# Performance work log

Hardware: AMD Instinct MI355X
Metric: run time of the kernel (lower is better)

Reference implementation:

```python
import jax, jax.numpy as jnp
import numpy as np
import math

N_H = 16
REL_K = 16  # relative-position clamp window


def setup_inputs() -> dict:
    key = jax.random.key(0)
    ks = jax.random.split(key, 7)
    B, S, D = 8, 1024, 1024
    d_k = D // N_H
    scale = 0.02
    return {
        "x": jax.random.normal(ks[0], (B, S, D), dtype=jnp.float32),
        "W_attn": jax.random.normal(ks[1], (D, 3 * D), dtype=jnp.float32) * scale,
        "b_attn": jax.random.normal(ks[2], (3 * D,), dtype=jnp.float32) * scale,
        "W_proj": jax.random.normal(ks[3], (D, D), dtype=jnp.float32) * scale,
        "b_proj": jax.random.normal(ks[4], (D,), dtype=jnp.float32) * scale,
        "lut_k": jax.random.normal(ks[5], (2 * REL_K + 1, d_k), dtype=jnp.float32) * scale,
        "lut_v": jax.random.normal(ks[6], (2 * REL_K + 1, d_k), dtype=jnp.float32) * scale,
    }


def reference(x, W_attn, b_attn, W_proj, b_proj, lut_k, lut_v):
    B, S, D = x.shape
    d_k = D // N_H

    qkv = x @ W_attn + b_attn  # [B, S, 3D]
    q, k, v = jnp.split(qkv, 3, axis=-1)
    # [B, H, S, d_k]
    q = q.reshape(B, S, N_H, d_k).transpose(0, 2, 1, 3)
    k = k.reshape(B, S, N_H, d_k).transpose(0, 2, 1, 3)
    v = v.reshape(B, S, N_H, d_k).transpose(0, 2, 1, 3)

    i = jnp.arange(S)[:, None]
    j = jnp.arange(S)[None, :]
    rel = jnp.clip(j - i, -REL_K, REL_K) + REL_K  # [S, S] in [0, 2k]
    aij_k = lut_k[rel]  # [S, S, d_k]
    aij_v = lut_v[rel]  # [S, S, d_k]

    scores = jnp.einsum('bhid,bhjd->bhij', q, k)
    scores = scores + jnp.einsum('bhid,ijd->bhij', q, aij_k)
    scores = scores * (1.0 / math.sqrt(d_k))

    causal = j <= i  # [S, S]
    scores = jnp.where(causal[None, None, :, :], scores, -jnp.inf)
    attn = jax.nn.softmax(scores, axis=-1)  # [B, H, S, S]

    out = jnp.einsum('bhij,bhjd->bhid', attn, v)
    out = out + jnp.einsum('bhij,ijd->bhid', attn, aij_v)
    out = out.transpose(0, 2, 1, 3).reshape(B, S, D)
    return out @ W_proj + b_proj
```

## Files before the change

### kernel.cpp

```cpp
#include <hip/hip_runtime.h>
#include <hip/hip_bf16.h>
#include <math.h>

#define NH 16
#define S_LEN 1024
#define DK 64
#define D_MODEL 1024
#define HSZ 8388608

typedef __attribute__((ext_vector_type(8))) short bf16x8;
typedef __attribute__((ext_vector_type(4))) float f32x4;
typedef unsigned short USH;

#define EXPSCALE 0.1803368801111204f

__device__ __forceinline__ float fast_exp2(float x) {
    return __builtin_amdgcn_exp2f(x);
}

__device__ __forceinline__ short f2b(float x) {
    union { __hip_bfloat16 h; short s; } u;
    u.h = __float2bfloat16(x);
    return u.s;
}
__device__ __forceinline__ float b2f(USH u) {
    union { unsigned i; float f; } x;
    x.i = (unsigned)u << 16;
    return x.f;
}

__device__ __forceinline__ void gload16(const void* src, void* lds) {
    __builtin_amdgcn_global_load_lds(
        (const __attribute__((address_space(1))) void*)src,
        (__attribute__((address_space(3))) void*)lds,
        16, 0, 0);
}

__global__ __launch_bounds__(256)
void conv_bf16_kernel(const float* __restrict__ in, USH* __restrict__ out) {
    const int i = (blockIdx.x * 256 + threadIdx.x) * 8;
    const float4 a = *(const float4*)&in[i];
    const float4 b = *(const float4*)&in[i + 4];
    ushort4 o0, o1;
    o0.x = (USH)f2b(a.x); o0.y = (USH)f2b(a.y); o0.z = (USH)f2b(a.z); o0.w = (USH)f2b(a.w);
    o1.x = (USH)f2b(b.x); o1.y = (USH)f2b(b.y); o1.z = (USH)f2b(b.z); o1.w = (USH)f2b(b.w);
    *(ushort4*)&out[i] = o0;
    *(ushort4*)&out[i + 4] = o1;
}

__global__ __launch_bounds__(256)
void transp_bf16_kernel(const float* __restrict__ in, USH* __restrict__ out,
                        int R, int C) {
    __shared__ USH Ts[64][65];
    const int r0 = blockIdx.y * 64, c0 = blockIdx.x * 64;
    const int tr = threadIdx.x >> 4;
    const int tc4 = (threadIdx.x & 15) * 4;
    #pragma unroll
    for (int ph = 0; ph < 4; ++ph) {
        const int r = ph * 16 + tr;
        const float4 v = *(const float4*)&in[(size_t)(r0 + r) * C + c0 + tc4];
        Ts[tc4 + 0][r] = (USH)f2b(v.x);
        Ts[tc4 + 1][r] = (USH)f2b(v.y);
        Ts[tc4 + 2][r] = (USH)f2b(v.z);
        Ts[tc4 + 3][r] = (USH)f2b(v.w);
    }
    __syncthreads();
    #pragma unroll
    for (int ph = 0; ph < 4; ++ph) {
        const int cc = ph * 16 + tr;
        ushort4 o;
        o.x = Ts[cc][tc4 + 0]; o.y = Ts[cc][tc4 + 1];
        o.z = Ts[cc][tc4 + 2]; o.w = Ts[cc][tc4 + 3];
        *(ushort4*)&out[(size_t)(c0 + cc) * R + r0 + tc4] = o;
    }
}

__global__ __launch_bounds__(256)
void vtransp_kernel(const USH* __restrict__ in, USH* __restrict__ out) {
    __shared__ USH T[64][72];
    const int bh = blockIdx.x >> 4;
    const int s0 = (blockIdx.x & 15) * 64;
    const int r = threadIdx.x >> 4;
    const int c4 = (threadIdx.x & 15) * 4;
    #pragma unroll
    for (int ph = 0; ph < 4; ++ph) {
        const int row = ph * 16 + r;
        const ushort4 v = *(const ushort4*)
            &in[((size_t)bh * S_LEN + s0 + row) * DK + c4];
        T[row][c4 + 0] = v.x; T[row][c4 + 1] = v.y;
        T[row][c4 + 2] = v.z; T[row][c4 + 3] = v.w;
    }
    __syncthreads();
    #pragma unroll
    for (int ph = 0; ph < 4; ++ph) {
        const int d = ph * 16 + r;
        ushort4 o;
        o.x = T[c4 + 0][d]; o.y = T[c4 + 1][d];
        o.z = T[c4 + 2][d]; o.w = T[c4 + 3][d];
        *(ushort4*)&out[(size_t)bh * (S_LEN * DK) + (size_t)d * S_LEN + s0 + c4] = o;
    }
}

template<int QKV>
__global__ __launch_bounds__(256)
void mfma_gemm_kernel(const USH* __restrict__ A, const USH* __restrict__ Bt,
                      const float* __restrict__ bias,
                      float* __restrict__ Cf, USH* __restrict__ Cq,
                      USH* __restrict__ Ck, USH* __restrict__ Cv,
                      int M, int N, int K) {
    __shared__ __align__(16) USH As[128 * 32];
    __shared__ __align__(16) USH Bs[128 * 32];
    const int t = threadIdx.x;
    const int w = t >> 6, lane = t & 63, g = lane >> 4, c = lane & 15;
    const int wm = w >> 1, wn = w & 1;
    const int bm0 = blockIdx.y * 128, bn0 = blockIdx.x * 128;

    const int sk = ((t & 3) ^ ((t >> 3) & 3)) * 8;
    const USH* pa0 = A + (size_t)(bm0 + (t >> 2)) * K + sk;
    const USH* pa1 = pa0 + (size_t)64 * K;
    const USH* pb0 = Bt + (size_t)(bn0 + (t >> 2)) * K + sk;
    const USH* pb1 = pb0 + (size_t)64 * K;
    USH* ldsA0 = &As[(t & ~63) * 8];
    USH* ldsA1 = ldsA0 + 2048;
    USH* ldsB0 = &Bs[(t & ~63) * 8];
    USH* ldsB1 = ldsB0 + 2048;

    unsigned aoff[4], boff[4];
    #pragma unroll
    for (int i = 0; i < 4; ++i) {
        const int r = wm * 64 + i * 16 + c;
        aoff[i] = ((unsigned)(r * 64 + g * 16)) ^ ((((unsigned)r >> 1) & 3) << 4);
        const int n = wn * 64 + i * 16 + c;
        boff[i] = ((unsigned)(n * 64 + g * 16)) ^ ((((unsigned)n >> 1) & 3) << 4);
    }

    f32x4 acc[4][4];
    #pragma unroll
    for (int i = 0; i < 4; ++i)
        #pragma unroll
        for (int j = 0; j < 4; ++j) acc[i][j] = (f32x4)0.f;

    for (int k0 = 0; k0 < K; k0 += 32) {
        gload16(pa0 + k0, ldsA0);
        gload16(pa1 + k0, ldsA1);
        gload16(pb0 + k0, ldsB0);
        gload16(pb1 + k0, ldsB1);
        __syncthreads();

        bf16x8 af[4], bfr[4];
        #pragma unroll
        for (int i = 0; i < 4; ++i) af[i] = *(const bf16x8*)((const char*)As + aoff[i]);
        #pragma unroll
        for (int j = 0; j < 4; ++j) bfr[j] = *(const bf16x8*)((const char*)Bs + boff[j]);
        #pragma unroll
        for (int i = 0; i < 4; ++i)
            #pragma unroll
            for (int j = 0; j < 4; ++j)
                acc[i][j] = __builtin_amdgcn_mfma_f32_16x16x32_bf16(
                    af[i], bfr[j], acc[i][j], 0, 0, 0);
        __syncthreads();
    }

    #pragma unroll
    for (int i = 0; i < 4; ++i) {
        #pragma unroll
        for (int reg = 0; reg < 4; ++reg) {
            const int m = bm0 + wm * 64 + i * 16 + g * 4 + reg;
            #pragma unroll
            for (int j = 0; j < 4; ++j) {
                const int n = bn0 + wn * 64 + j * 16 + c;
                const float v = acc[i][j][reg] + bias[n];
                if (QKV) {
                    const int which = n >> 10;
                    const int h = (n & 1023) >> 6, d = n & 63;
                    const int b = m >> 10, s = m & 1023;
                    const size_t idx = (((size_t)(b * NH + h)) * S_LEN + s) * DK + d;
                    if (which == 0)      Cq[idx] = (USH)f2b(v);
                    else if (which == 1) Ck[idx] = (USH)f2b(v);
                    else                 Cv[idx] = (USH)f2b(v);
                } else {
                    Cf[(size_t)m * N + n] = v;
                }
            }
        }
    }
}

__global__ __launch_bounds__(512, 4)
void attn_mfma_kernel(const USH* __restrict__ qb,
                      const USH* __restrict__ kbuf,
                      const USH* __restrict__ vtg,
                      const float* __restrict__ lut_k,
                      const float* __restrict__ lut_v,
                      USH* __restrict__ ao) {
    const int bid = blockIdx.x;
    const int logical = (bid & 7) * 128 + (bid >> 3);
    const int ib = 7 - (logical & 7);
    const int bh = logical >> 3;
    const int b = bh >> 4, h = bh & 15;
    const int i0 = ib * 128;
    const int t = threadIdx.x;
    const int w = t >> 6;
    const int lane = t & 63;
    const int g = lane >> 4;
    const int c = lane & 15;

    __shared__ __align__(16) char smem[64640];
    char* pb    = smem + 32768;
    char* qsb   = smem + 32768;
    char* lutkb = smem + 56448;
    USH* qrelb  = (USH*)(smem + 49152);
    USH* lvfb   = (USH*)(smem + 54272);
    float* tapss = (float*)(smem + 56448);

    const USH* qp  = qb   + (size_t)bh * (S_LEN * DK);
    const USH* kp  = kbuf + (size_t)bh * (S_LEN * DK);
    const USH* vtp = vtg  + (size_t)bh * (S_LEN * DK);

    auto stage = [&](int j0, int koff, int voff) {
        const int o = t * 16;
        const int row = o >> 7;
        const int chunk = (o >> 4) & 7;
        const int sc = (chunk ^ (row & 7)) * 8;
        gload16(kp + (size_t)(j0 + row) * DK + sc, smem + koff + o);
        gload16(vtp + (size_t)row * S_LEN + j0 + sc, smem + voff + o);
    };

    stage(0, 0, 16384);
    for (int f = t; f < 2048; f += 512) {
        const int row = f >> 4, c4 = (f & 15) * 4;
        unsigned byte = ((unsigned)(row * 128 + c4 * 2)) ^ (((unsigned)row & 7) << 4);
        *(ushort4*)(qsb + byte) = *(const ushort4*)&qp[(size_t)(i0 + row) * DK + c4];
    }
    for (int e = t; e < 32 * 64; e += 512) {
        const int row = e >> 6, d = e & 63;
        const USH v = (row < 17) ? (USH)f2b(lut_k[row * 64 + d]) : (USH)0;
        unsigned byte = ((unsigned)(row * 128 + d * 2)) ^ (((unsigned)row & 7) << 4);
        *(USH*)(lutkb + byte) = v;
    }
    for (int e = t; e < 17 * 64; e += 512)
        lvfb[e] = (USH)f2b(lut_v[e]);
    __syncthreads();

    bf16x8 qa[2];
    {
        const int row = w * 16 + c;
        #pragma unroll
        for (int kh = 0; kh < 2; ++kh) {
            unsigned byte = ((unsigned)(row * 128 + kh * 64 + g * 16))
                          ^ (((unsigned)row & 7) << 4);
            qa[kh] = *(const bf16x8*)(qsb + byte);
        }
    }

    {
        f32x4 qr[2];
        qr[0] = (f32x4)0.f; qr[1] = (f32x4)0.f;
        #pragma unroll
        for (int sub2 = 0; sub2 < 2; ++sub2) {
            const int tap = sub2 * 16 + c;
            #pragma unroll
            for (int kh = 0; kh < 2; ++kh) {
                unsigned byte = ((unsigned)(tap * 128 + kh * 64 + g * 16))
                              ^ (((unsigned)tap & 7) << 4);
                bf16x8 lb = *(const bf16x8*)(lutkb + byte);
                qr[sub2] = __builtin_amdgcn_mfma_f32_16x16x32_bf16(
                    qa[kh], lb, qr[sub2], 0, 0, 0);
            }
        }
        #pragma unroll
        for (int sub2 = 0; sub2 < 2; ++sub2) {
            const int tap = sub2 * 16 + c;
            if (tap < 17) {
                #pragma unroll
                for (int r = 0; r < 4; ++r)
                    qrelb[(w * 16 + g * 4 + r) * 20 + tap] = (USH)f2b(qr[sub2][r]);
            }
        }
    }
    __syncthreads();

    float qrel0s[4];
    #pragma unroll
    for (int r = 0; r < 4; ++r)
        qrel0s[r] = b2f(qrelb[(w * 16 + g * 4 + r) * 20]) * EXPSCALE;

    f32x4 acc[4];
    #pragma unroll
    for (int dt = 0; dt < 4; ++dt) acc[dt] = (f32x4)0.f;
    float l_r[4];
    #pragma unroll
    for (int r = 0; r < 4; ++r) l_r[r] = 0.f;

    const int wrow0 = i0 + w * 16;
    const int NT = 2 * ib + 2;
    for (int tile = 0; tile < NT; ++tile) {
        const int cur = tile & 1;
        if (tile + 1 < NT)
            stage((tile + 1) << 6, cur ? 0 : 8192, cur ? 16384 : 24576);

        if (tile * 64 > wrow0 + 15) {
            __syncthreads();
            continue;
        }

        const char* ktb = smem + (cur ? 8192 : 0);
        const char* vtb = smem + (cur ? 24576 : 16384);

        float p[4][4];
        __builtin_amdgcn_s_setprio(1);
        f32x4 s[4];
        #pragma unroll
        for (int sub = 0; sub < 4; ++sub) {
            s[sub] = (f32x4)0.f;
            const int krow = sub * 16 + c;
            #pragma unroll
            for (int kh = 0; kh < 2; ++kh) {
                unsigned byte = ((unsigned)krow << 7) + ((unsigned)kh << 6) + ((unsigned)g << 4);
                byte ^= (unsigned)(krow & 7) << 4;
                bf16x8 kb = *(const bf16x8*)(ktb + byte);
                s[sub] = __builtin_amdgcn_mfma_f32_16x16x32_bf16(qa[kh], kb, s[sub], 0, 0, 0);
            }
        }
        __builtin_amdgcn_s_setprio(0);

        if (tile * 64 + 79 <= wrow0) {
            #pragma unroll
            for (int sub = 0; sub < 4; ++sub)
                #pragma unroll
                for (int r = 0; r < 4; ++r)
                    p[sub][r] = fast_exp2(s[sub][r] * EXPSCALE + qrel0s[r]);
        } else {
            #pragma unroll
            for (int sub = 0; sub < 4; ++sub) {
                const int dbase = tile * 64 + (sub * 16 + c) - i0 - (w * 16 + g * 4);
                #pragma unroll
                for (int r = 0; r < 4; ++r) {
                    const int dj = dbase - r;
                    int t17 = dj + 16;
                    t17 = t17 < 0 ? 0 : (t17 > 16 ? 16 : t17);
                    const int il = w * 16 + g * 4 + r;
                    float pv = fast_exp2((s[sub][r] + b2f(qrelb[il * 20 + t17])) * EXPSCALE);
                    if (dj > 0) pv = 0.f;
                    p[sub][r] = pv;
                    if (dj >= -15 && dj <= 0)
                        tapss[il * 16 + dj + 15] = pv;
                }
            }
        }

        #pragma unroll
        for (int r = 0; r < 4; ++r)
            l_r[r] += (p[0][r] + p[1][r]) + (p[2][r] + p[3][r]);

        char* pw = pb + w * 2048;
        #pragma unroll
        for (int sub = 0; sub < 4; ++sub)
            #pragma unroll
            for (int r = 0; r < 4; ++r) {
                const int row = g * 4 + r;
                unsigned byte = ((unsigned)row << 7) + (((unsigned)(sub * 16 + c)) << 1);
                byte ^= (unsigned)(row & 7) << 4;
                *(short*)(pw + byte) = f2b(p[sub][r]);
            }

        bf16x8 pa[2];
        #pragma unroll
        for (int jh = 0; jh < 2; ++jh) {
            unsigned byte = ((unsigned)c << 7) + ((unsigned)jh << 6) + ((unsigned)g << 4);
            byte ^= (unsigned)(c & 7) << 4;
            pa[jh] = *(const bf16x8*)(pw + byte);
        }
        __builtin_amdgcn_s_setprio(1);
        #pragma unroll
        for (int dt = 0; dt < 4; ++dt) {
            const int d = dt * 16 + c;
            #pragma unroll
            for (int jh = 0; jh < 2; ++jh) {
                unsigned byte = ((unsigned)d << 7) + ((unsigned)jh << 6) + ((unsigned)g << 4);
                byte ^= (unsigned)(d & 7) << 4;
                bf16x8 vb = *(const bf16x8*)(vtb + byte);
                acc[dt] = __builtin_amdgcn_mfma_f32_16x16x32_bf16(pa[jh], vb, acc[dt], 0, 0, 0);
            }
        }
        __builtin_amdgcn_s_setprio(0);
        __syncthreads();
    }

    const int rbase = w * 16 + g * 4;
    #pragma unroll
    for (int r = 0; r < 4; ++r) {
        float lsum = l_r[r];
        #pragma unroll
        for (int msk = 1; msk < 16; msk <<= 1)
            lsum += __shfl_xor(lsum, msk);
        const int il = rbase + r;
        float c0 = lsum;
        float tp[16];
        #pragma unroll
        for (int tap = 0; tap < 16; ++tap) {
            const int jg = i0 + il + tap - 15;
            const float pv = (jg >= 0) ? tapss[il * 16 + tap] : 0.f;
            tp[tap] = pv;
            c0 -= pv;
        }
        const float invl = 1.f / lsum;
        #pragma unroll
        for (int dt = 0; dt < 4; ++dt) {
            const int d = dt * 16 + c;
            float o = acc[dt][r] + c0 * b2f(lvfb[d]);
            #pragma unroll
            for (int tap = 0; tap < 16; ++tap)
                o += tp[tap] * b2f(lvfb[(tap + 1) * 64 + d]);
            o *= invl;
            ao[((size_t)b * S_LEN + (i0 + il)) * D_MODEL + h * DK + d] = (USH)f2b(o);
        }
    }
}

extern "C" void kernel_launch(void* const* d_in, const int* in_sizes, int n_in,
                              void* d_out, int out_size, void* d_ws, size_t ws_size,
                              hipStream_t stream) {
    const float* x      = (const float*)d_in[0];
    const float* W_attn = (const float*)d_in[1];
    const float* b_attn = (const float*)d_in[2];
    const float* W_proj = (const float*)d_in[3];
    const float* b_proj = (const float*)d_in[4];
    const float* lut_k  = (const float*)d_in[5];
    const float* lut_v  = (const float*)d_in[6];
    float* out = (float*)d_out;

    USH* qb    = (USH*)d_ws;
    USH* kb    = qb + HSZ;
    USH* vb    = kb + HSZ;
    USH* vtg   = vb + HSZ;
    USH* aob   = vtg + HSZ;
    USH* xb    = aob + HSZ;
    USH* watt  = xb + HSZ;
    USH* wproj = watt + 3145728;

    conv_bf16_kernel<<<HSZ / (256 * 8), 256, 0, stream>>>(x, xb);
    transp_bf16_kernel<<<dim3(3072 / 64, 1024 / 64), 256, 0, stream>>>(
        W_attn, watt, 1024, 3072);
    transp_bf16_kernel<<<dim3(1024 / 64, 1024 / 64), 256, 0, stream>>>(
        W_proj, wproj, 1024, 1024);

    mfma_gemm_kernel<1><<<dim3(3072 / 128, 8192 / 128), 256, 0, stream>>>(
        xb, watt, b_attn, nullptr, qb, kb, vb, 8192, 3072, 1024);

    vtransp_kernel<<<2048, 256, 0, stream>>>(vb, vtg);

    attn_mfma_kernel<<<1024, 512, 0, stream>>>(qb, kb, vtg, lut_k, lut_v, aob);

    mfma_gemm_kernel<0><<<dim3(1024 / 128, 8192 / 128), 256, 0, stream>>>(
        aob, wproj, b_proj, out, nullptr, nullptr, nullptr, 8192, 1024, 1024);
}
```

Before: 207.0 us.

## Shrink attention LDS footprint by halving P staging and storing taps in bf16

Cuts the shared memory per block from about 63KB to about 51KB. It does this by staging P in two 32-column halves (a 1KB per-wave buffer instead of 2KB), storing the diagonal tap probabilities as bf16 instead of fp32, and overlapping the LUT region with the unused K buffer. The lut_v load is moved into registers before the first barrier and written to LDS after it, so it can alias the reused region. The aim is to fit more workgroups per CU. The cost is an extra LDS round trip per half and some precision loss on the tap values.

```diff
diff --git a/kernel.cpp b/kernel.cpp
--- a/kernel.cpp
+++ b/kernel.cpp
@@ -205,13 +205,13 @@
     const int g = lane >> 4;
     const int c = lane & 15;
 
-    __shared__ __align__(16) char smem[64640];
-    char* pb    = smem + 32768;
-    char* qsb   = smem + 32768;
-    char* lutkb = smem + 56448;
-    USH* qrelb  = (USH*)(smem + 49152);
-    USH* lvfb   = (USH*)(smem + 54272);
-    float* tapss = (float*)(smem + 56448);
+    __shared__ __align__(16) char smem[52352];
+    char* pb     = smem + 32768;
+    char* qsb    = smem + 32768;
+    char* lutkb  = smem + 8192;
+    USH* qrelb   = (USH*)(smem + 40960);
+    USH* lvfb    = (USH*)(smem + 46080);
+    USH* tapssb  = (USH*)(smem + 48256);
 
     const USH* qp  = qb   + (size_t)bh * (S_LEN * DK);
     const USH* kp  = kbuf + (size_t)bh * (S_LEN * DK);
@@ -238,8 +238,9 @@
         unsigned byte = ((unsigned)(row * 128 + d * 2)) ^ (((unsigned)row & 7) << 4);
         *(USH*)(lutkb + byte) = v;
     }
-    for (int e = t; e < 17 * 64; e += 512)
-        lvfb[e] = (USH)f2b(lut_v[e]);
+    const float lv0f = lut_v[t];
+    const float lv1f = lut_v[t + 512];
+    const float lv2f = (t + 1024 < 1088) ? lut_v[t + 1024] : 0.f;
     __syncthreads();
 
     bf16x8 qa[2];
@@ -253,32 +254,34 @@
         }
     }
 
-    {
-        f32x4 qr[2];
-        qr[0] = (f32x4)0.f; qr[1] = (f32x4)0.f;
-        #pragma unroll
-        for (int sub2 = 0; sub2 < 2; ++sub2) {
-            const int tap = sub2 * 16 + c;
-            #pragma unroll
-            for (int kh = 0; kh < 2; ++kh) {
-                unsigned byte = ((unsigned)(tap * 128 + kh * 64 + g * 16))
-                              ^ (((unsigned)tap & 7) << 4);
-                bf16x8 lb = *(const bf16x8*)(lutkb + byte);
-                qr[sub2] = __builtin_amdgcn_mfma_f32_16x16x32_bf16(
-                    qa[kh], lb, qr[sub2], 0, 0, 0);
-            }
-        }
-        #pragma unroll
-        for (int sub2 = 0; sub2 < 2; ++sub2) {
-            const int tap = sub2 * 16 + c;
-            if (tap < 17) {
-                #pragma unroll
-                for (int r = 0; r < 4; ++r)
-                    qrelb[(w * 16 + g * 4 + r) * 20 + tap] = (USH)f2b(qr[sub2][r]);
-            }
+    f32x4 qr[2];
+    qr[0] = (f32x4)0.f; qr[1] = (f32x4)0.f;
+    #pragma unroll
+    for (int sub2 = 0; sub2 < 2; ++sub2) {
+        const int tap = sub2 * 16 + c;
+        #pragma unroll
+        for (int kh = 0; kh < 2; ++kh) {
+            unsigned byte = ((unsigned)(tap * 128 + kh * 64 + g * 16))
+                          ^ (((unsigned)tap & 7) << 4);
+            bf16x8 lb = *(const bf16x8*)(lutkb + byte);
+            qr[sub2] = __builtin_amdgcn_mfma_f32_16x16x32_bf16(
+                qa[kh], lb, qr[sub2], 0, 0, 0);
         }
     }
     __syncthreads();
+
+    #pragma unroll
+    for (int sub2 = 0; sub2 < 2; ++sub2) {
+        const int tap = sub2 * 16 + c;
+        if (tap < 17) {
+            #pragma unroll
+            for (int r = 0; r < 4; ++r)
+                qrelb[(w * 16 + g * 4 + r) * 20 + tap] = (USH)f2b(qr[sub2][r]);
+        }
+    }
+    lvfb[t] = (USH)f2b(lv0f);
+    lvfb[t + 512] = (USH)f2b(lv1f);
+    if (t + 1024 < 1088) lvfb[t + 1024] = (USH)f2b(lv2f);
 
     float qrel0s[4];
     #pragma unroll
@@ -344,7 +347,7 @@
                     if (dj > 0) pv = 0.f;
                     p[sub][r] = pv;
                     if (dj >= -15 && dj <= 0)
-                        tapss[il * 16 + dj + 15] = pv;
+                        tapssb[il * 16 + dj + 15] = (USH)f2b(pv);
                 }
             }
         }
@@ -353,37 +356,34 @@
         for (int r = 0; r < 4; ++r)
             l_r[r] += (p[0][r] + p[1][r]) + (p[2][r] + p[3][r]);
 
-        char* pw = pb + w * 2048;
-        #pragma unroll
-        for (int sub = 0; sub < 4; ++sub)
-            #pragma unroll
-            for (int r = 0; r < 4; ++r) {
-                const int row = g * 4 + r;
-                unsigned byte = ((unsigned)row << 7) + (((unsigned)(sub * 16 + c)) << 1);
-                byte ^= (unsigned)(row & 7) << 4;
-                *(short*)(pw + byte) = f2b(p[sub][r]);
+        char* pw = pb + w * 1024;
+        #pragma unroll
+        for (int half = 0; half < 2; ++half) {
+            #pragma unroll
+            for (int sh = 0; sh < 2; ++sh) {
+                const int sub = half * 2 + sh;
+                #pragma unroll
+                for (int r = 0; r < 4; ++r) {
+                    const int row = g * 4 + r;
+                    unsigned byte = (unsigned)(row * 64 + (sh * 16 + c) * 2);
+                    byte ^= (unsigned)(row & 3) << 4;
+                    *(short*)(pw + byte) = f2b(p[sub][r]);
+                }
             }
-
-        bf16x8 pa[2];
-        #pragma unroll
-        for (int jh = 0; jh < 2; ++jh) {
-            unsigned byte = ((unsigned)c << 7) + ((unsigned)jh << 6) + ((unsigned)g << 4);
-            byte ^= (unsigned)(c & 7) << 4;
-            pa[jh] = *(const bf16x8*)(pw + byte);
-        }
-        __builtin_amdgcn_s_setprio(1);
-        #pragma unroll
-        for (int dt = 0; dt < 4; ++dt) {
-            const int d = dt * 16 + c;
-            #pragma unroll
-            for (int jh = 0; jh < 2; ++jh) {
-                unsigned byte = ((unsigned)d << 7) + ((unsigned)jh << 6) + ((unsigned)g << 4);
-                byte ^= (unsigned)(d & 7) << 4;
-                bf16x8 vb = *(const bf16x8*)(vtb + byte);
-                acc[dt] = __builtin_amdgcn_mfma_f32_16x16x32_bf16(pa[jh], vb, acc[dt], 0, 0, 0);
+            unsigned pbyte = ((unsigned)c * 64 + (unsigned)g * 16)
+                           ^ (((unsigned)c & 3) << 4);
+            bf16x8 pa = *(const bf16x8*)(pw + pbyte);
+            __builtin_amdgcn_s_setprio(1);
+            #pragma unroll
+            for (int dt = 0; dt < 4; ++dt) {
+                const int d = dt * 16 + c;
+                unsigned vbyte = ((unsigned)d << 7) + ((unsigned)half << 6) + ((unsigned)g << 4);
+                vbyte ^= (unsigned)(d & 7) << 4;
+                bf16x8 vb = *(const bf16x8*)(vtb + vbyte);
+                acc[dt] = __builtin_amdgcn_mfma_f32_16x16x32_bf16(pa, vb, acc[dt], 0, 0, 0);
             }
-        }
-        __builtin_amdgcn_s_setprio(0);
+            __builtin_amdgcn_s_setprio(0);
+        }
         __syncthreads();
     }
 
@@ -400,7 +400,7 @@
         #pragma unroll
         for (int tap = 0; tap < 16; ++tap) {
             const int jg = i0 + il + tap - 15;
-            const float pv = (jg >= 0) ? tapss[il * 16 + tap] : 0.f;
+            const float pv = (jg >= 0) ? b2f(tapssb[il * 16 + tap]) : 0.f;
             tp[tap] = pv;
             c0 -= pv;
         }
```

New measurement: 210.9 us. Within noise of the previous version (+1.9%).

## Triple-buffer K/V tiles with prefetch distance two and vmcnt waits

Applied to the files above, without the earlier changes.

Moves the K/V staging from double to triple buffering, prefetching two tiles ahead and using explicit s_waitcnt vmcnt plus raw s_barrier instead of __syncthreads. The goal is to hide global load latency and avoid full-drain barriers each tile. Tap probabilities are now stored in LDS as bf16 rather than fp32 so the larger shared memory layout fits. This raises LDS use to about 77KB per block, which may reduce occupancy, and slightly lowers the precision of the tap correction.

```diff
diff --git a/kernel.cpp b/kernel.cpp
--- a/kernel.cpp
+++ b/kernel.cpp
@@ -205,28 +205,28 @@
     const int g = lane >> 4;
     const int c = lane & 15;
 
-    __shared__ __align__(16) char smem[64640];
-    char* pb    = smem + 32768;
-    char* qsb   = smem + 32768;
-    char* lutkb = smem + 56448;
-    USH* qrelb  = (USH*)(smem + 49152);
-    USH* lvfb   = (USH*)(smem + 54272);
-    float* tapss = (float*)(smem + 56448);
+    __shared__ __align__(16) char smem[76928];
+    char* pb     = smem + 49152;
+    char* qsb    = smem + 49152;
+    char* lutkb  = smem + 8192;
+    USH* qrelb   = (USH*)(smem + 65536);
+    USH* lvfb    = (USH*)(smem + 70656);
+    USH* tapssb  = (USH*)(smem + 72832);
 
     const USH* qp  = qb   + (size_t)bh * (S_LEN * DK);
     const USH* kp  = kbuf + (size_t)bh * (S_LEN * DK);
     const USH* vtp = vtg  + (size_t)bh * (S_LEN * DK);
 
-    auto stage = [&](int j0, int koff, int voff) {
+    auto stage = [&](int j0, int slot) {
         const int o = t * 16;
         const int row = o >> 7;
         const int chunk = (o >> 4) & 7;
         const int sc = (chunk ^ (row & 7)) * 8;
-        gload16(kp + (size_t)(j0 + row) * DK + sc, smem + koff + o);
-        gload16(vtp + (size_t)row * S_LEN + j0 + sc, smem + voff + o);
+        gload16(kp + (size_t)(j0 + row) * DK + sc, smem + slot * 8192 + o);
+        gload16(vtp + (size_t)row * S_LEN + j0 + sc, smem + 24576 + slot * 8192 + o);
     };
 
-    stage(0, 0, 16384);
+    stage(0, 0);
     for (int f = t; f < 2048; f += 512) {
         const int row = f >> 4, c4 = (f & 15) * 4;
         unsigned byte = ((unsigned)(row * 128 + c4 * 2)) ^ (((unsigned)row & 7) << 4);
@@ -278,13 +278,16 @@
             }
         }
     }
-    __syncthreads();
-
     float qrel0s[4];
     #pragma unroll
     for (int r = 0; r < 4; ++r)
         qrel0s[r] = b2f(qrelb[(w * 16 + g * 4 + r) * 20]) * EXPSCALE;
 
+    __syncthreads();
+
+    const int NT = 2 * ib + 2;
+    if (1 < NT) stage(64, 1);
+
     f32x4 acc[4];
     #pragma unroll
     for (int dt = 0; dt < 4; ++dt) acc[dt] = (f32x4)0.f;
@@ -293,19 +296,23 @@
     for (int r = 0; r < 4; ++r) l_r[r] = 0.f;
 
     const int wrow0 = i0 + w * 16;
-    const int NT = 2 * ib + 2;
+    int cur = 0;
     for (int tile = 0; tile < NT; ++tile) {
-        const int cur = tile & 1;
-        if (tile + 1 < NT)
-            stage((tile + 1) << 6, cur ? 0 : 8192, cur ? 16384 : 24576);
+        const int nxt2 = tile + 2;
+        const int slot2 = (cur + 2 >= 3) ? cur - 1 : cur + 2;
+        if (nxt2 < NT)
+            stage(nxt2 << 6, slot2);
 
         if (tile * 64 > wrow0 + 15) {
-            __syncthreads();
+            if (nxt2 < NT) asm volatile("s_waitcnt vmcnt(2)" ::: "memory");
+            else           asm volatile("s_waitcnt vmcnt(0)" ::: "memory");
+            __builtin_amdgcn_s_barrier();
+            cur = (cur + 1 == 3) ? 0 : cur + 1;
             continue;
         }
 
-        const char* ktb = smem + (cur ? 8192 : 0);
-        const char* vtb = smem + (cur ? 24576 : 16384);
+        const char* ktb = smem + cur * 8192;
+        const char* vtb = smem + 24576 + cur * 8192;
 
         float p[4][4];
         __builtin_amdgcn_s_setprio(1);
@@ -344,7 +351,7 @@
                     if (dj > 0) pv = 0.f;
                     p[sub][r] = pv;
                     if (dj >= -15 && dj <= 0)
-                        tapss[il * 16 + dj + 15] = pv;
+                        tapssb[il * 16 + dj + 15] = (USH)f2b(pv);
                 }
             }
         }
@@ -384,7 +391,11 @@
             }
         }
         __builtin_amdgcn_s_setprio(0);
-        __syncthreads();
+
+        if (nxt2 < NT) asm volatile("s_waitcnt vmcnt(2)" ::: "memory");
+        else           asm volatile("s_waitcnt vmcnt(0)" ::: "memory");
+        __builtin_amdgcn_s_barrier();
+        cur = (cur + 1 == 3) ? 0 : cur + 1;
     }
 
     const int rbase = w * 16 + g * 4;
@@ -400,7 +411,7 @@
         #pragma unroll
         for (int tap = 0; tap < 16; ++tap) {
             const int jg = i0 + il + tap - 15;
-            const float pv = (jg >= 0) ? tapss[il * 16 + tap] : 0.f;
+            const float pv = (jg >= 0) ? b2f(tapssb[il * 16 + tap]) : 0.f;
             tp[tap] = pv;
             c0 -= pv;
         }
```

New measurement: 208.0 us. Within noise of the previous version (+0.5%).
